# Optimization experiments

Measured on AMD Instinct MI355X. Metric: run time of the kernel, lower is better.

## Reference

```python
import jax, jax.numpy as jnp
import numpy as np

INPUT_SIZE = 416.0
CONF_THRESH = 0.25
IOU_THRESH = 0.45
N = 8192


def setup_inputs() -> dict:
    key = jax.random.key(0)
    preds = jax.random.normal(key, (1, 5, N), dtype=jnp.float32)
    return {"preds": preds}


def _pairwise_iou(b):
    # b: [N,4] xyxy -> iou: [N,N], matching the torch clamp(min=0) semantics
    xx1 = jnp.maximum(b[:, None, 0], b[None, :, 0])
    yy1 = jnp.maximum(b[:, None, 1], b[None, :, 1])
    xx2 = jnp.minimum(b[:, None, 2], b[None, :, 2])
    yy2 = jnp.minimum(b[:, None, 3], b[None, :, 3])
    inter = jnp.clip(xx2 - xx1, 0.0) * jnp.clip(yy2 - yy1, 0.0)
    area = jnp.clip(b[:, 2] - b[:, 0], 0.0) * jnp.clip(b[:, 3] - b[:, 1], 0.0)  # [N]
    union = area[:, None] + area[None, :] - inter
    return jnp.where(union > 0, inter / union, 0.0)


def reference(preds):
    # decode: preds [1,5,N] rows = (cx, cy, w, h, obj)
    p = preds[0].T  # [N,5]
    cx, cy, pw, ph, obj = p[:, 0], p[:, 1], p[:, 2], p[:, 3], p[:, 4]
    x1 = cx - pw * 0.5
    y1 = cy - ph * 0.5
    x2 = cx + pw * 0.5
    y2 = cy + ph * 0.5
    boxes = jnp.stack([x1, y1, x2, y2], axis=1)  # [N,4]
    scores = obj
    classes = jnp.zeros_like(scores)

    valid = scores > CONF_THRESH  # conf filter (kept as mask; invalid boxes never kept)
    # scale to absolute coords iff all coords are normalized (max <= 1)
    scale = jnp.where(jnp.max(boxes) <= 1.0, INPUT_SIZE, 1.0)
    boxes_abs = boxes * scale

    # greedy NMS over score-descending order
    order = jnp.argsort(-scores)
    b = boxes_abs[order]          # [N,4]
    s = scores[order]             # [N]
    v = valid[order]              # [N]
    c = classes[order]            # [N]

    iou = _pairwise_iou(b)        # [N,N]

    def step(suppressed, xs):
        iou_row, v_i, i = xs
        keep_i = v_i & jnp.logical_not(suppressed[i])
        suppressed = suppressed | (keep_i & (iou_row > IOU_THRESH))
        return suppressed, keep_i

    _, keep = jax.lax.scan(
        step,
        jnp.zeros((N,), dtype=bool),
        (iou, v, jnp.arange(N)),
    )  # keep: [N] bool, in sorted order

    out = jnp.stack(
        [b[:, 0] / INPUT_SIZE, b[:, 1] / INPUT_SIZE,
         b[:, 2] / INPUT_SIZE, b[:, 3] / INPUT_SIZE, s, c],
        axis=1,
    )  # [N,6]
    # fixed-shape jit-compatible output: suppressed/filtered rows are zeroed;
    # kept rows appear in descending-score order (same order torch compacts to)
    return jnp.where(keep[:, None], out, 0.0)
```

## Files before the change

### kernel.cpp

```cpp
#include <hip/hip_runtime.h>
#include <stdint.h>

typedef unsigned long long u64;
typedef unsigned int u32;

#define NBOX 8192
#define ACMAX 1024
#define NCH 16
#define CONF 0.25f
#define IOU_T 0.45f

#define OFF_CNT    0
#define OFF_CX1    256
#define OFF_CY1    (OFF_CX1 + ACMAX * 4)
#define OFF_CX2    (OFF_CX1 + 2 * ACMAX * 4)
#define OFF_CY2    (OFF_CX1 + 3 * ACMAX * 4)
#define OFF_CSC    (OFF_CX1 + 4 * ACMAX * 4)
#define OFF_CAR    (OFF_CX1 + 5 * ACMAX * 4)
#define OFF_ROFC   (OFF_CX1 + 6 * ACMAX * 4)
#define OFF_CMASKT (OFF_CX1 + 7 * ACMAX * 4)

__device__ inline u64 readlane64(u64 v, int l) {
    u32 lo = (u32)__builtin_amdgcn_readlane((int)(u32)v, l);
    u32 hi = (u32)__builtin_amdgcn_readlane((int)(u32)(v >> 32), l);
    return ((u64)hi << 32) | (u64)lo;
}

__device__ inline u32 encf(float f) {
    u32 u = __float_as_uint(f);
    return (u & 0x80000000u) ? ~u : (u | 0x80000000u);
}

__global__ void __launch_bounds__(1024) k_sort(
        const float* __restrict__ p,
        float* __restrict__ cx1, float* __restrict__ cy1,
        float* __restrict__ cx2, float* __restrict__ cy2,
        float* __restrict__ csc, float* __restrict__ car,
        int* __restrict__ rofc, u32* __restrict__ cnt0,
        float* __restrict__ out) {
    #pragma clang fp contract(off)
    int t = threadIdx.x;
    int b = blockIdx.x;
    __shared__ u64 keys[1024];
    __shared__ u32 accs[128][36];
    __shared__ u32 accs2[8][32];
    __shared__ float redm[16];
    __shared__ float s_gmax;

    if (b == 0 && t == 0) *cnt0 = 0u;

    int il4 = (t & 7) * 4;
    int js  = t >> 3;
    int ibase = b * 32;

    u64 Ki[4];
    #pragma unroll
    for (int q = 0; q < 4; q++) {
        int i = ibase + il4 + q;
        u32 e = encf(p[4 * NBOX + i]);
        Ki[q] = ((u64)e << 32) | ((u64)(8191 - i) << 19) | 0x1FFFFull;
    }

    u32 acc[4] = {0u, 0u, 0u, 0u};
    float mloc = -3.4e38f;
    for (int w = 0; w < 8; w++) {
        int j = w * 1024 + t;
        float cxj = p[j], cyj = p[NBOX + j];
        float pwj = p[2 * NBOX + j], phj = p[3 * NBOX + j];
        float sj = p[4 * NBOX + j];
        float hx = pwj * 0.5f, hy = phj * 0.5f;
        float x1 = cxj - hx, y1 = cyj - hy, x2 = cxj + hx, y2 = cyj + hy;
        bool act = (sj > CONF) && (x2 > x1) && (y2 > y1);
        mloc = fmaxf(mloc, fmaxf(fmaxf(x1, y1), fmaxf(x2, y2)));
        u32 e = encf(sj);
        u32 mult = act ? 65537u : 1u;
        __syncthreads();
        keys[t] = ((u64)e << 32) | ((u64)(8191 - j) << 19) | (u64)mult;
        __syncthreads();
        int base = js * 8;
        #pragma unroll
        for (int k2 = 0; k2 < 4; k2++) {
            u64 ka = keys[base + k2 * 2];
            u64 kb = keys[base + k2 * 2 + 1];
            u32 ma = (u32)ka & 0x1FFFFu;
            u32 mb = (u32)kb & 0x1FFFFu;
            #pragma unroll
            for (int q = 0; q < 4; q++) {
                acc[q] += (ka > Ki[q]) ? ma : 0u;
                acc[q] += (kb > Ki[q]) ? mb : 0u;
            }
        }
    }
    #pragma unroll
    for (int q = 0; q < 4; q++) accs[js][il4 + q] = acc[q];
    #pragma unroll
    for (int o = 32; o > 0; o >>= 1) mloc = fmaxf(mloc, __shfl_xor(mloc, o, 64));
    if ((t & 63) == 0) redm[t >> 6] = mloc;
    __syncthreads();
    if (t < 256) {
        int il = t & 31, part = t >> 5;
        u32 s = 0;
        #pragma unroll
        for (int q = 0; q < 16; q++) s += accs[part * 16 + q][il];
        accs2[part][il] = s;
    }
    if (t == 0) {
        float g = redm[0];
        #pragma unroll
        for (int k = 1; k < 16; k++) g = fmaxf(g, redm[k]);
        s_gmax = g;
    }
    __syncthreads();
    if (t < 32) {
        u32 total = 0;
        #pragma unroll
        for (int part = 0; part < 8; part++) total += accs2[part][t];
        int r = (int)(total & 0xFFFFu);
        int cr = (int)(total >> 16);
        int i = ibase + t;
        float scale = (s_gmax <= 1.0f) ? 416.0f : 1.0f;
        float cx = p[i], cy = p[NBOX + i];
        float pw = p[2 * NBOX + i], ph = p[3 * NBOX + i];
        float s = p[4 * NBOX + i];
        float hx = pw * 0.5f, hy = ph * 0.5f;
        float x1 = cx - hx, y1 = cy - hy, x2 = cx + hx, y2 = cy + hy;
        bool a = (s > CONF) && (x2 > x1) && (y2 > y1);
        float bx1 = x1 * scale, by1 = y1 * scale;
        float bx2 = x2 * scale, by2 = y2 * scale;
        float aw = fmaxf(bx2 - bx1, 0.0f);
        float ah = fmaxf(by2 - by1, 0.0f);
        float area = aw * ah;
        bool ok = a && (cr < ACMAX);
        if (ok) {
            cx1[cr] = bx1; cy1[cr] = by1; cx2[cr] = bx2; cy2[cr] = by2;
            csc[cr] = s; car[cr] = area; rofc[cr] = r;
        } else {
            bool valid = s > CONF;
            float* o = out + (size_t)r * 6;
            o[0] = valid ? bx1 / 416.0f : 0.0f;
            o[1] = valid ? by1 / 416.0f : 0.0f;
            o[2] = valid ? bx2 / 416.0f : 0.0f;
            o[3] = valid ? by2 / 416.0f : 0.0f;
            o[4] = valid ? s : 0.0f;
            o[5] = 0.0f;
        }
    }
}

__global__ void __launch_bounds__(1024) k_nms2(
        const float* __restrict__ cx1, const float* __restrict__ cy1,
        const float* __restrict__ cx2, const float* __restrict__ cy2,
        const float* __restrict__ car, const float* __restrict__ csc,
        const int* __restrict__ rofc, u64* __restrict__ cmaskT,
        u32* __restrict__ cnt, float* __restrict__ out) {
    #pragma clang fp contract(off)
    int t = threadIdx.x;
    int ci = blockIdx.x;
    __shared__ float sx1[64], sy1[64], sx2[64], sy2[64], sa[64];
    __shared__ u64 keptArr[NCH];
    __shared__ int isLast;

    if (t < 64) {
        sx1[t] = cx1[ci * 64 + t]; sy1[t] = cy1[ci * 64 + t];
        sx2[t] = cx2[ci * 64 + t]; sy2[t] = cy2[ci * 64 + t];
        sa[t]  = car[ci * 64 + t];
    }
    __syncthreads();
    float xj1 = cx1[t], yj1 = cy1[t], xj2 = cx2[t], yj2 = cy2[t];
    float aj = car[t];
    float s = csc[t];
    {
        u64 w = 0;
        for (int ii = 0; ii < 64; ii++) {
            float xx1 = fmaxf(sx1[ii], xj1);
            float yy1 = fmaxf(sy1[ii], yj1);
            float xx2 = fminf(sx2[ii], xj2);
            float yy2 = fminf(sy2[ii], yj2);
            float iw = fmaxf(xx2 - xx1, 0.0f);
            float ih = fmaxf(yy2 - yy1, 0.0f);
            float inter = iw * ih;
            float uni = sa[ii] + aj - inter;
            bool sup = (uni > 0.0f) && (inter / uni > IOU_T);
            w |= ((u64)(sup ? 1u : 0u)) << ii;
        }
        cmaskT[(size_t)ci * ACMAX + t] = w;
    }
    __threadfence();
    __syncthreads();
    if (t == 0) {
        u32 old = __hip_atomic_fetch_add(cnt, 1u, __ATOMIC_ACQ_REL,
                                         __HIP_MEMORY_SCOPE_AGENT);
        isLast = (old == (u32)(NCH - 1)) ? 1 : 0;
    }
    __syncthreads();
    if (!isLast) return;
    __threadfence();

    int wv = t >> 6;
    bool valid = s > CONF;
    u64 col[NCH];
    #pragma unroll
    for (int w = 0; w < NCH; w++) col[w] = cmaskT[(size_t)w * ACMAX + t];
    bool sup = false;
    for (int c = 0; c < NCH; c++) {
        if (wv == c) {
            u64 validm = __ballot(valid);
            u64 supm = __ballot(sup);
            u64 d = col[c];
            u64 kept = 0;
            u64 cand = validm & ~supm;
            while (cand) {
                int i = __builtin_ctzll(cand);
                kept |= (1ull << i);
                u64 row = readlane64(d, i);
                u64 gt = (i < 63) ? (~0ull << (i + 1)) : 0ull;
                cand = cand & ~row & gt;
            }
            if ((t & 63) == 0) keptArr[c] = kept;
        }
        __syncthreads();
        u64 k = keptArr[c];
        if (wv > c && (col[c] & k) != 0ull) sup = true;
    }
    __syncthreads();
    if (valid) {
        bool kb = (keptArr[t >> 6] >> (t & 63)) & 1ull;
        int r = rofc[t];
        float* o = out + (size_t)r * 6;
        o[0] = kb ? xj1 / 416.0f : 0.0f;
        o[1] = kb ? yj1 / 416.0f : 0.0f;
        o[2] = kb ? xj2 / 416.0f : 0.0f;
        o[3] = kb ? yj2 / 416.0f : 0.0f;
        o[4] = kb ? s : 0.0f;
        o[5] = 0.0f;
    }
}

extern "C" void kernel_launch(void* const* d_in, const int* in_sizes, int n_in,
                              void* d_out, int out_size, void* d_ws, size_t ws_size,
                              hipStream_t stream) {
    const float* preds = (const float*)d_in[0];
    float* out = (float*)d_out;
    char* ws = (char*)d_ws;
    u32* cnt   = (u32*)(ws + OFF_CNT);
    float* cx1 = (float*)(ws + OFF_CX1);
    float* cy1 = (float*)(ws + OFF_CY1);
    float* cx2 = (float*)(ws + OFF_CX2);
    float* cy2 = (float*)(ws + OFF_CY2);
    float* csc = (float*)(ws + OFF_CSC);
    float* car = (float*)(ws + OFF_CAR);
    int* rofc  = (int*)(ws + OFF_ROFC);
    u64* cmaskT = (u64*)(ws + OFF_CMASKT);

    hipLaunchKernelGGL(k_sort, dim3(256), dim3(1024), 0, stream,
                       preds, cx1, cy1, cx2, cy2, csc, car, rofc, cnt, out);
    hipLaunchKernelGGL(k_nms2, dim3(NCH), dim3(1024), 0, stream,
                       cx1, cy1, cx2, cy2, car, csc, rofc, cmaskT, cnt, out);
}
```

Baseline: 111.2 us.

## Run final greedy NMS resolve in a single wavefront without block barriers

The last-arriving block's serial NMS resolve now runs in one 64-lane wavefront instead of 16 wavefronts synchronising through shared memory with __syncthreads per chunk. Each lane loops over all 16 chunks, computing suppression from earlier chunks' kept masks by reading the transposed mask words directly, so no block barriers are needed. The intent is to remove 16 barrier rounds and idle waves from the serial tail. In exchange a single wave issues more global loads per lane and handles all output writes itself.

```diff
diff --git a/kernel.cpp b/kernel.cpp
--- a/kernel.cpp
+++ b/kernel.cpp
@@ -157,7 +157,6 @@
     int t = threadIdx.x;
     int ci = blockIdx.x;
     __shared__ float sx1[64], sy1[64], sx2[64], sy2[64], sa[64];
-    __shared__ u64 keptArr[NCH];
     __shared__ int isLast;
 
     if (t < 64) {
@@ -166,10 +165,9 @@
         sa[t]  = car[ci * 64 + t];
     }
     __syncthreads();
-    float xj1 = cx1[t], yj1 = cy1[t], xj2 = cx2[t], yj2 = cy2[t];
-    float aj = car[t];
-    float s = csc[t];
     {
+        float xj1 = cx1[t], yj1 = cy1[t], xj2 = cx2[t], yj2 = cy2[t];
+        float aj = car[t];
         u64 w = 0;
         for (int ii = 0; ii < 64; ii++) {
             float xx1 = fmaxf(sx1[ii], xj1);
@@ -194,45 +192,64 @@
     }
     __syncthreads();
     if (!isLast) return;
+    if (t >= 64) return;
     __threadfence();
 
-    int wv = t >> 6;
-    bool valid = s > CONF;
-    u64 col[NCH];
-    #pragma unroll
-    for (int w = 0; w < NCH; w++) col[w] = cmaskT[(size_t)w * ACMAX + t];
-    bool sup = false;
-    for (int c = 0; c < NCH; c++) {
-        if (wv == c) {
-            u64 validm = __ballot(valid);
-            u64 supm = __ballot(sup);
-            u64 d = col[c];
-            u64 kept = 0;
-            u64 cand = validm & ~supm;
-            while (cand) {
-                int i = __builtin_ctzll(cand);
-                kept |= (1ull << i);
-                u64 row = readlane64(d, i);
-                u64 gt = (i < 63) ? (~0ull << (i + 1)) : 0ull;
-                cand = cand & ~row & gt;
-            }
-            if ((t & 63) == 0) keptArr[c] = kept;
-        }
-        __syncthreads();
-        u64 k = keptArr[c];
-        if (wv > c && (col[c] & k) != 0ull) sup = true;
-    }
-    __syncthreads();
-    if (valid) {
-        bool kb = (keptArr[t >> 6] >> (t & 63)) & 1ull;
-        int r = rofc[t];
-        float* o = out + (size_t)r * 6;
-        o[0] = kb ? xj1 / 416.0f : 0.0f;
-        o[1] = kb ? yj1 / 416.0f : 0.0f;
-        o[2] = kb ? xj2 / 416.0f : 0.0f;
-        o[3] = kb ? yj2 / 416.0f : 0.0f;
-        o[4] = kb ? s : 0.0f;
-        o[5] = 0.0f;
+    int l = t;
+    float sc[NCH];
+    u32 validb = 0;
+    #pragma unroll
+    for (int c2 = 0; c2 < NCH; c2++) {
+        sc[c2] = csc[c2 * 64 + l];
+        validb |= (sc[c2] > CONF ? 1u : 0u) << c2;
+    }
+    u64 diag[NCH];
+    #pragma unroll
+    for (int c = 0; c < NCH; c++)
+        diag[c] = cmaskT[(size_t)c * ACMAX + c * 64 + l];
+
+    u32 keptv = 0;
+    u64 keptU[NCH];
+    #pragma unroll
+    for (int c2 = 0; c2 < NCH; c2++) {
+        u64 hit = 0;
+        #pragma unroll
+        for (int c = 0; c < c2; c++) {
+            u64 wq = cmaskT[(size_t)c * ACMAX + c2 * 64 + l];
+            hit |= (wq & keptU[c]);
+        }
+        bool suppd = hit != 0ull;
+        u64 validm = __ballot((validb >> c2) & 1u);
+        u64 supm   = __ballot(suppd);
+        u64 d = diag[c2];
+        u64 kept = 0;
+        u64 cand = validm & ~supm;
+        while (cand) {
+            int i = __builtin_ctzll(cand);
+            kept |= (1ull << i);
+            u64 row = readlane64(d, i);
+            u64 gt = (i < 63) ? (~0ull << (i + 1)) : 0ull;
+            cand = cand & ~row & gt;
+        }
+        keptU[c2] = kept;
+        keptv |= (u32)((kept >> l) & 1ull) << c2;
+    }
+    #pragma unroll
+    for (int c2 = 0; c2 < NCH; c2++) {
+        int j = c2 * 64 + l;
+        float s = sc[c2];
+        if (s > CONF) {
+            bool kb = (keptv >> c2) & 1u;
+            int r = rofc[j];
+            float bx1 = cx1[j], by1 = cy1[j], bx2 = cx2[j], by2 = cy2[j];
+            float* o = out + (size_t)r * 6;
+            o[0] = kb ? bx1 / 416.0f : 0.0f;
+            o[1] = kb ? by1 / 416.0f : 0.0f;
+            o[2] = kb ? bx2 / 416.0f : 0.0f;
+            o[3] = kb ? by2 / 416.0f : 0.0f;
+            o[4] = kb ? s : 0.0f;
+            o[5] = 0.0f;
+        }
     }
 }
 
```

Measured after the change: 120.3 us. 8.2% more time.
